# Kernel optimization log

Hardware: AMD Instinct MI355X
Metric: run time of the kernel (lower is better)

## Reference

```python
import jax, jax.numpy as jnp
import numpy as np

N = 50000      # nodes
E = 400000     # edges (before self-loops)
G = 256        # graphs in batch
H = 2          # attention heads
C = 100        # out channels per head
F_IN = 336
SLOPE = 0.2    # PyG GATConv default negative_slope


def setup_inputs() -> dict:
    key = jax.random.key(0)
    ks = jax.random.split(key, 32)
    inp = {}
    inp['x'] = jax.random.normal(ks[0], (N, F_IN), dtype=jnp.float32)
    inp['edge_index'] = jax.random.randint(ks[1], (2, E), 0, N, dtype=jnp.int32)
    inp['batch'] = jnp.sort(jax.random.randint(ks[2], (N,), 0, G, dtype=jnp.int32))
    dims = [F_IN, 200, 200, 200, 200]
    k = 3
    for i in range(5):
        d = dims[i]
        inp[f'W{i+1}'] = jax.random.normal(ks[k], (d, H * C), dtype=jnp.float32) / float(np.sqrt(d)); k += 1
        inp[f'asrc{i+1}'] = jax.random.normal(ks[k], (H, C), dtype=jnp.float32) * 0.1; k += 1
        inp[f'adst{i+1}'] = jax.random.normal(ks[k], (H, C), dtype=jnp.float32) * 0.1; k += 1
        inp[f'bc{i+1}'] = jnp.zeros((H * C,), jnp.float32)
    for i, (a, b) in enumerate([(200, 100), (100, 100), (100, 29)]):
        inp[f'lw{i+1}'] = jax.random.normal(ks[k], (a, b), dtype=jnp.float32) / float(np.sqrt(a)); k += 1
        inp[f'lb{i+1}'] = jnp.zeros((b,), jnp.float32)
    return inp


def _gat(x, src, dst, W, a_s, a_d, b):
    # PyG GATConv (concat=True): per-head linear, additive attention,
    # softmax over incoming edges per destination node, weighted sum.
    h = (x @ W).reshape(-1, H, C)                      # [N,H,C]
    es = jnp.einsum('nhc,hc->nh', h, a_s)              # [N,H] src scores
    ed = jnp.einsum('nhc,hc->nh', h, a_d)              # [N,H] dst scores
    e = jax.nn.leaky_relu(es[src] + ed[dst], SLOPE)    # [E+N,H]
    m = jax.ops.segment_max(e, dst, num_segments=N)    # per-dest max (stable softmax)
    p = jnp.exp(e - m[dst])
    s = jax.ops.segment_sum(p, dst, num_segments=N)
    alpha = p / (s[dst] + 1e-16)                       # [E+N,H]
    msg = alpha[:, :, None] * h[src]                   # [E+N,H,C]
    out = jax.ops.segment_sum(msg, dst, num_segments=N)
    return out.reshape(-1, H * C) + b


def reference(x, edge_index, batch,
              W1, asrc1, adst1, bc1, W2, asrc2, adst2, bc2,
              W3, asrc3, adst3, bc3, W4, asrc4, adst4, bc4,
              W5, asrc5, adst5, bc5,
              lw1, lb1, lw2, lb2, lw3, lb3):
    loop = jnp.arange(N, dtype=edge_index.dtype)       # self-loops (PyG default)
    src = jnp.concatenate([edge_index[0], loop])
    dst = jnp.concatenate([edge_index[1], loop])
    for W, a_s, a_d, b in [(W1, asrc1, adst1, bc1), (W2, asrc2, adst2, bc2),
                           (W3, asrc3, adst3, bc3), (W4, asrc4, adst4, bc4),
                           (W5, asrc5, adst5, bc5)]:
        x = jax.nn.relu(_gat(x, src, dst, W, a_s, a_d, b))
    # global mean pool over nodes of each graph
    sums = jax.ops.segment_sum(x, batch, num_segments=G)
    cnt = jax.ops.segment_sum(jnp.ones((N, 1), x.dtype), batch, num_segments=G)
    x = sums / jnp.maximum(cnt, 1.0)
    x = jax.nn.relu(x @ lw1 + lb1)
    x = jax.nn.relu(x @ lw2 + lb2)
    return x @ lw3 + lb3
```

## Files before the change

### kernel.cpp

```cpp
#include <hip/hip_runtime.h>
#include <hip/hip_bf16.h>
#include <math.h>

#define F_IN   336
#define HC     200
#define Cch    100
#define SLOPE  0.2f
#define SCAN_BS 256

#define NPAD   224
#define KP0    352
#define KP1    224

using short8   = __attribute__((ext_vector_type(8))) short;
using float4v  = __attribute__((ext_vector_type(4))) float;
using ushort4v = __attribute__((ext_vector_type(4))) unsigned short;
using float2v  = __attribute__((ext_vector_type(2))) float;

typedef __attribute__((address_space(1))) const void GASV;
typedef __attribute__((address_space(3))) void LASV;

__device__ inline unsigned short rne_bf16(float v) {
    unsigned int u = __float_as_uint(v);
    return (unsigned short)((u + 0x7fffu + ((u >> 16) & 1u)) >> 16);
}
__device__ inline void split_bf(float v, unsigned short& hi, unsigned short& lo) {
    hi = rne_bf16(v);
    float hv = __uint_as_float(((unsigned int)hi) << 16);
    lo = rne_bf16(v - hv);
}

__device__ inline unsigned int enc_f32(float f) {
    unsigned int u = __float_as_uint(f);
    return (u & 0x80000000u) ? ~u : (u | 0x80000000u);
}
__device__ inline float dec_f32(unsigned int e) {
    return __uint_as_float((e & 0x80000000u) ? (e ^ 0x80000000u) : ~e);
}

__global__ void init_deg(int* deg, unsigned int* gmax, int n) {
    int i = blockIdx.x * 256 + threadIdx.x;
    if (i < n) deg[i] = 1;
    if (i < 10) gmax[i] = 0x007FFFFFu;
}

__global__ void count_deg(const int* __restrict__ dst, int* deg, int e) {
    int i = blockIdx.x * 256 + threadIdx.x;
    if (i < e) atomicAdd(&deg[dst[i]], 1);
}

__global__ void scan_block(const int* __restrict__ deg, int* incl, int* bsums, int n) {
    __shared__ int sm[SCAN_BS];
    int i = blockIdx.x * SCAN_BS + threadIdx.x;
    int v = (i < n) ? deg[i] : 0;
    sm[threadIdx.x] = v;
    __syncthreads();
    for (int off = 1; off < SCAN_BS; off <<= 1) {
        int t = (threadIdx.x >= off) ? sm[threadIdx.x - off] : 0;
        __syncthreads();
        sm[threadIdx.x] += t;
        __syncthreads();
    }
    if (i < n) incl[i] = sm[threadIdx.x];
    if (threadIdx.x == SCAN_BS - 1) bsums[blockIdx.x] = sm[threadIdx.x];
}

__global__ void scan_sums(int* bsums, int nb) {
    __shared__ int sm[SCAN_BS];
    int v = (threadIdx.x < nb) ? bsums[threadIdx.x] : 0;
    sm[threadIdx.x] = v;
    __syncthreads();
    for (int off = 1; off < SCAN_BS; off <<= 1) {
        int t = (threadIdx.x >= off) ? sm[threadIdx.x - off] : 0;
        __syncthreads();
        sm[threadIdx.x] += t;
        __syncthreads();
    }
    if (threadIdx.x < nb) bsums[threadIdx.x] = sm[threadIdx.x] - v;
}

__global__ void scan_final(const int* __restrict__ incl, const int* __restrict__ deg,
                           const int* __restrict__ bsums, int* row_ptr, int* cursor, int n) {
    int i = blockIdx.x * SCAN_BS + threadIdx.x;
    if (i < n) {
        int inc = incl[i] + bsums[i / SCAN_BS];
        int ex  = inc - deg[i];
        row_ptr[i] = ex;
        cursor[i]  = ex;
        if (i == n - 1) row_ptr[n] = inc;
    }
}

__global__ void fill_csr(const int* __restrict__ src, const int* __restrict__ dst,
                         int* cursor, int* col_src, int e, int n) {
    int i = blockIdx.x * 256 + threadIdx.x;
    int te = e + n;
    if (i >= te) return;
    int s, d;
    if (i < e) { s = src[i]; d = dst[i]; }
    else       { s = i - e;  d = i - e; }
    int pos = atomicAdd(&cursor[d], 1);
    col_src[pos] = s;
}

__global__ void conv_x(const float* __restrict__ x, unsigned short* __restrict__ Ah,
                       unsigned short* __restrict__ Al, int n_nodes) {
    const int GPR = KP0 / 4;
    int i = blockIdx.x * 256 + threadIdx.x;
    int tot = n_nodes * GPR;
    if (i >= tot) return;
    int row = i / GPR, g4 = i - row * GPR;
    int col = g4 * 4;
    float4v v = {0.f, 0.f, 0.f, 0.f};
    if (col < F_IN) v = *(const float4v*)(x + (size_t)row * F_IN + col);
    ushort4v hv, lv;
    split_bf(v.x, ((unsigned short*)&hv)[0], ((unsigned short*)&lv)[0]);
    split_bf(v.y, ((unsigned short*)&hv)[1], ((unsigned short*)&lv)[1]);
    split_bf(v.z, ((unsigned short*)&hv)[2], ((unsigned short*)&lv)[2]);
    split_bf(v.w, ((unsigned short*)&hv)[3], ((unsigned short*)&lv)[3]);
    size_t b = (size_t)row * KP0 + col;
    *(ushort4v*)(Ah + b) = hv;
    *(ushort4v*)(Al + b) = lv;
}

__global__ void conv_w_all(const float* __restrict__ W0, const float* __restrict__ W1,
                           const float* __restrict__ W2, const float* __restrict__ W3,
                           const float* __restrict__ W4,
                           unsigned short* __restrict__ Bh, unsigned short* __restrict__ Bl) {
    const int SZ0 = NPAD * KP0, SZ = NPAD * KP1;
    const int TOT = SZ0 + 4 * SZ;
    int i = blockIdx.x * 256 + threadIdx.x;
    if (i >= TOT) return;
    const float* W; int Kp, K, idx;
    if (i < SZ0) { W = W0; Kp = KP0; K = F_IN; idx = i; }
    else {
        int j = i - SZ0; int l = j / SZ; idx = j - l * SZ;
        W = (l == 0) ? W1 : (l == 1) ? W2 : (l == 2) ? W3 : W4;
        Kp = KP1; K = HC;
    }
    int n = idx / Kp, k = idx - n * Kp;
    float v = (n < HC && k < K) ? W[(size_t)k * HC + n] : 0.f;
    unsigned short hi, lo;
    split_bf(v, hi, lo);
    Bh[i] = hi; Bl[i] = lo;
}

#define LBUF 18432
__global__ __launch_bounds__(256, 2) void gemm_split(
    const unsigned short* __restrict__ Ah, const unsigned short* __restrict__ Al,
    const unsigned short* __restrict__ Bh, const unsigned short* __restrict__ Bl,
    const float* __restrict__ asrc, const float* __restrict__ adst,
    float* __restrict__ h, float* __restrict__ es, float* __restrict__ ed,
    unsigned int* __restrict__ gmax,
    int M, int Kp)
{
    __shared__ unsigned short Ls[2][LBUF];
    __shared__ float sc[64][4];
    int tid  = threadIdx.x;
    int wave = tid >> 6, lane = tid & 63;
    int quad = lane >> 4, l16 = lane & 15;
    int wm = (wave >> 1) * 32;
    int wn = (wave & 1) * 112;
    int r0 = blockIdx.x * 64;

    ((float*)sc)[tid] = 0.f;

    const unsigned short* gp[9];
    unsigned lof[9];
    {
        int r16 = lane >> 2;
        int cl  = (lane & 3) ^ ((lane >> 3) & 3);
#pragma unroll
        for (int j = 0; j < 9; j++) {
            int c = wave * 9 + j;
            if (c < 8) {
                int s = c >> 2, rb = (c & 3) * 16;
                int gr = r0 + rb + r16; if (gr >= M) gr = M - 1;
                gp[j]  = (s ? Al : Ah) + (size_t)gr * Kp + cl * 8;
                lof[j] = s * 2048 + rb * 32;
            } else {
                int cb = c - 8;
                int s = (cb >= 14) ? 1 : 0, rb = (cb - s * 14) * 16;
                gp[j]  = (s ? Bl : Bh) + (size_t)(rb + r16) * Kp + cl * 8;
                lof[j] = 4096 + s * 7168 + rb * 32;
            }
        }
    }

    float4v acc[2][7];
#pragma unroll
    for (int mt = 0; mt < 2; mt++)
#pragma unroll
        for (int nt = 0; nt < 7; nt++)
            acc[mt][nt] = (float4v){0.f, 0.f, 0.f, 0.f};

#pragma unroll
    for (int j = 0; j < 9; j++)
        __builtin_amdgcn_global_load_lds((GASV*)(gp[j]), (LASV*)(&Ls[0][0] + lof[j]), 16, 0, 0);
    __syncthreads();

    for (int k0 = 0; k0 < Kp; k0 += 32) {
        int cur = (k0 >> 5) & 1;
        int kn  = k0 + 32;
        if (kn < Kp) {
            unsigned short* lb = &Ls[cur ^ 1][0];
#pragma unroll
            for (int j = 0; j < 9; j++)
                __builtin_amdgcn_global_load_lds((GASV*)(gp[j] + kn), (LASV*)(lb + lof[j]), 16, 0, 0);
        }

        const unsigned short* Lc = &Ls[cur][0];
        short8 a_h[2], a_l[2];
#pragma unroll
        for (int mt = 0; mt < 2; mt++) {
            int row = wm + mt * 16 + l16;
            int cph = (quad ^ ((row >> 1) & 3)) * 8;
            a_h[mt] = *(const short8*)(Lc + row * 32 + cph);
            a_l[mt] = *(const short8*)(Lc + 2048 + row * 32 + cph);
        }
#pragma unroll
        for (int nt = 0; nt < 7; nt++) {
            int row = wn + nt * 16 + l16;
            int cph = (quad ^ ((row >> 1) & 3)) * 8;
            short8 b_h = *(const short8*)(Lc + 4096 + row * 32 + cph);
            short8 b_l = *(const short8*)(Lc + 11264 + row * 32 + cph);
#pragma unroll
            for (int mt = 0; mt < 2; mt++) {
                acc[mt][nt] = __builtin_amdgcn_mfma_f32_16x16x32_bf16(a_h[mt], b_h, acc[mt][nt], 0, 0, 0);
                acc[mt][nt] = __builtin_amdgcn_mfma_f32_16x16x32_bf16(a_h[mt], b_l, acc[mt][nt], 0, 0, 0);
                acc[mt][nt] = __builtin_amdgcn_mfma_f32_16x16x32_bf16(a_l[mt], b_h, acc[mt][nt], 0, 0, 0);
            }
        }
        __syncthreads();
    }

    float asc[7], adc[7];
    bool  vld[7];
    bool  hd1[7];
#pragma unroll
    for (int nt = 0; nt < 7; nt++) {
        int col = wn + nt * 16 + l16;
        vld[nt] = col < HC;
        hd1[nt] = col >= Cch;
        asc[nt] = vld[nt] ? asrc[col] : 0.f;
        adc[nt] = vld[nt] ? adst[col] : 0.f;
    }

#pragma unroll
    for (int mt = 0; mt < 2; mt++) {
        float p[4][4];
#pragma unroll
        for (int r = 0; r < 4; r++)
#pragma unroll
            for (int t = 0; t < 4; t++) p[r][t] = 0.f;
#pragma unroll
        for (int nt = 0; nt < 7; nt++) {
            int col = wn + nt * 16 + l16;
#pragma unroll
            for (int r = 0; r < 4; r++) {
                float v = acc[mt][nt][r];
                int grow = r0 + wm + mt * 16 + quad * 4 + r;
                if (vld[nt] && grow < M) h[(size_t)grow * HC + col] = v;
                float va = v * asc[nt], vd = v * adc[nt];
                p[r][0] += hd1[nt] ? 0.f : va;
                p[r][1] += hd1[nt] ? va  : 0.f;
                p[r][2] += hd1[nt] ? 0.f : vd;
                p[r][3] += hd1[nt] ? vd  : 0.f;
            }
        }
#pragma unroll
        for (int off = 1; off < 16; off <<= 1)
#pragma unroll
            for (int r = 0; r < 4; r++)
#pragma unroll
                for (int t = 0; t < 4; t++)
                    p[r][t] += __shfl_xor(p[r][t], off);
        if (l16 == 0) {
            int lrow = wm + mt * 16 + quad * 4;
#pragma unroll
            for (int r = 0; r < 4; r++)
#pragma unroll
                for (int t = 0; t < 4; t++)
                    atomicAdd(&sc[lrow + r][t], p[r][t]);
        }
    }
    __syncthreads();
    if (tid < 64) {
        int grow = r0 + tid;
        bool v = grow < M;
        float e0v = v ? sc[tid][0] : -INFINITY;
        float e1v = v ? sc[tid][1] : -INFINITY;
        if (v) {
            es[grow * 2 + 0] = e0v;
            es[grow * 2 + 1] = e1v;
            ed[grow * 2 + 0] = sc[tid][2];
            ed[grow * 2 + 1] = sc[tid][3];
        }
#pragma unroll
        for (int off = 1; off < 64; off <<= 1) {
            e0v = fmaxf(e0v, __shfl_xor(e0v, off));
            e1v = fmaxf(e1v, __shfl_xor(e1v, off));
        }
        if (tid == 0) {
            atomicMax(&gmax[0], enc_f32(e0v));
            atomicMax(&gmax[1], enc_f32(e1v));
        }
    }
}

template<bool WF, bool WB>
__global__ __launch_bounds__(256) void gat_gather(
    const float* __restrict__ h, const float* __restrict__ es, const float* __restrict__ ed,
    const unsigned int* __restrict__ gmax,
    const int* __restrict__ row_ptr, const int* __restrict__ col_src,
    const float* __restrict__ bias, float* __restrict__ outF,
    unsigned short* __restrict__ oh, unsigned short* __restrict__ ol, int n_nodes)
{
    int wave = threadIdx.x >> 6, lane = threadIdx.x & 63;
    int n = blockIdx.x * 4 + wave;
    if (n >= n_nodes) return;
    int e0 = row_ptr[n], e1 = row_ptr[n + 1];
    bool act  = lane < 50;
    int  hsel = (lane >= 25) ? 1 : 0;
    float ed0 = ed[n * 2], ed1 = ed[n * 2 + 1];
    float gm0 = dec_f32(gmax[0]), gm1 = dec_f32(gmax[1]);
    float t0 = gm0 + ed0, t1 = gm1 + ed1;
    float mb0 = t0 > 0.f ? t0 : SLOPE * t0;
    float mb1 = t1 > 0.f ? t1 : SLOPE * t1;

    float l0 = 0.f, l1 = 0.f;
    float4v a0 = {0.f, 0.f, 0.f, 0.f}, a1 = {0.f, 0.f, 0.f, 0.f};
    float4v a2 = {0.f, 0.f, 0.f, 0.f}, a3 = {0.f, 0.f, 0.f, 0.f};

    for (int cbase = e0; cbase < e1; cbase += 64) {
        int cnt = e1 - cbase; if (cnt > 64) cnt = 64;
        int   sidx = 0;
        float px = 0.f, py = 0.f;
        if (lane < cnt) {
            sidx = col_src[cbase + lane];
            float2v q = *(const float2v*)&es[sidx * 2];
            float s0 = q.x + ed0, s1 = q.y + ed1;
            s0 = s0 > 0.f ? s0 : SLOPE * s0;
            s1 = s1 > 0.f ? s1 : SLOPE * s1;
            px = __expf(s0 - mb0);
            py = __expf(s1 - mb1);
            l0 += px; l1 += py;
        }
        int j = 0;
        for (; j + 4 <= cnt; j += 4) {
            int s0 = __shfl(sidx, j + 0), s1 = __shfl(sidx, j + 1);
            int s2 = __shfl(sidx, j + 2), s3 = __shfl(sidx, j + 3);
            float x0 = __shfl(px, j + 0), y0 = __shfl(py, j + 0);
            float x1 = __shfl(px, j + 1), y1 = __shfl(py, j + 1);
            float x2 = __shfl(px, j + 2), y2 = __shfl(py, j + 2);
            float x3 = __shfl(px, j + 3), y3 = __shfl(py, j + 3);
            float p0 = hsel ? y0 : x0;
            float p1 = hsel ? y1 : x1;
            float p2 = hsel ? y2 : x2;
            float p3 = hsel ? y3 : x3;
            if (act) {
                float4v v0 = *(const float4v*)(h + (size_t)s0 * HC + lane * 4);
                float4v v1 = *(const float4v*)(h + (size_t)s1 * HC + lane * 4);
                float4v v2 = *(const float4v*)(h + (size_t)s2 * HC + lane * 4);
                float4v v3 = *(const float4v*)(h + (size_t)s3 * HC + lane * 4);
                a0.x += p0 * v0.x; a0.y += p0 * v0.y; a0.z += p0 * v0.z; a0.w += p0 * v0.w;
                a1.x += p1 * v1.x; a1.y += p1 * v1.y; a1.z += p1 * v1.z; a1.w += p1 * v1.w;
                a2.x += p2 * v2.x; a2.y += p2 * v2.y; a2.z += p2 * v2.z; a2.w += p2 * v2.w;
                a3.x += p3 * v3.x; a3.y += p3 * v3.y; a3.z += p3 * v3.z; a3.w += p3 * v3.w;
            }
        }
        for (; j < cnt; j++) {
            int s0 = __shfl(sidx, j);
            float x0 = __shfl(px, j), y0 = __shfl(py, j);
            float p0 = hsel ? y0 : x0;
            if (act) {
                float4v v0 = *(const float4v*)(h + (size_t)s0 * HC + lane * 4);
                a0.x += p0 * v0.x; a0.y += p0 * v0.y; a0.z += p0 * v0.z; a0.w += p0 * v0.w;
            }
        }
    }
#pragma unroll
    for (int off = 1; off < 64; off <<= 1) {
        l0 += __shfl_xor(l0, off);
        l1 += __shfl_xor(l1, off);
    }

    float4v acc;
    acc.x = (a0.x + a1.x) + (a2.x + a3.x);
    acc.y = (a0.y + a1.y) + (a2.y + a3.y);
    acc.z = (a0.z + a1.z) + (a2.z + a3.z);
    acc.w = (a0.w + a1.w) + (a2.w + a3.w);

    float li = 1.f / ((hsel ? l1 : l0) + 1e-33f);
    if (act) {
        float4v bb = *(const float4v*)(bias + lane * 4);
        float4v r;
        r.x = fmaxf(acc.x * li + bb.x, 0.f);
        r.y = fmaxf(acc.y * li + bb.y, 0.f);
        r.z = fmaxf(acc.z * li + bb.z, 0.f);
        r.w = fmaxf(acc.w * li + bb.w, 0.f);
        if (WF) {
            __builtin_nontemporal_store(r, (float4v*)(outF + (size_t)n * HC + lane * 4));
        }
        if (WB) {
            ushort4v hv, lv;
            split_bf(r.x, ((unsigned short*)&hv)[0], ((unsigned short*)&lv)[0]);
            split_bf(r.y, ((unsigned short*)&hv)[1], ((unsigned short*)&lv)[1]);
            split_bf(r.z, ((unsigned short*)&hv)[2], ((unsigned short*)&lv)[2]);
            split_bf(r.w, ((unsigned short*)&hv)[3], ((unsigned short*)&lv)[3]);
            size_t b = (size_t)n * NPAD + lane * 4;
            __builtin_nontemporal_store(hv, (ushort4v*)(oh + b));
            __builtin_nontemporal_store(lv, (ushort4v*)(ol + b));
        }
    } else if (WB && lane < 56) {
        ushort4v z = {0, 0, 0, 0};
        size_t b = (size_t)n * NPAD + lane * 4;
        __builtin_nontemporal_store(z, (ushort4v*)(oh + b));
        __builtin_nontemporal_store(z, (ushort4v*)(ol + b));
    }
}

__global__ void bounds_zero(const int* __restrict__ batch, int* gstart,
                            float* pool, int n, int g) {
    int i = blockIdx.x * 256 + threadIdx.x;
    if (i < g * HC) pool[i] = 0.f;
    if (i >= n) return;
    int b = batch[i];
    int bp = (i == 0) ? -1 : batch[i - 1];
    for (int q = bp + 1; q <= b; q++) gstart[q] = i;
    if (i == n - 1) for (int q = b + 1; q <= g; q++) gstart[q] = n;
}

__global__ __launch_bounds__(256) void pool_part(
    const float* __restrict__ x, const int* __restrict__ batch,
    float* __restrict__ pool, int n_nodes)
{
    int wave = threadIdx.x >> 6, lane = threadIdx.x & 63;
    int base = (blockIdx.x * 4 + wave) * 16;
    if (base >= n_nodes) return;
    bool act = lane < 50;
    int end = base + 16; if (end > n_nodes) end = n_nodes;
    float4v acc = {0.f, 0.f, 0.f, 0.f};
    int curg = batch[base];
    for (int n = base; n < end; n++) {
        int g = batch[n];
        if (g != curg) {
            if (act) {
                float* pp = pool + (size_t)curg * HC + lane * 4;
                atomicAdd(pp + 0, acc.x); atomicAdd(pp + 1, acc.y);
                atomicAdd(pp + 2, acc.z); atomicAdd(pp + 3, acc.w);
            }
            acc = (float4v){0.f, 0.f, 0.f, 0.f};
            curg = g;
        }
        if (act) {
            float4v v = *(const float4v*)(x + (size_t)n * HC + lane * 4);
            acc.x += v.x; acc.y += v.y; acc.z += v.z; acc.w += v.w;
        }
    }
    if (act) {
        float* pp = pool + (size_t)curg * HC + lane * 4;
        atomicAdd(pp + 0, acc.x); atomicAdd(pp + 1, acc.y);
        atomicAdd(pp + 2, acc.z); atomicAdd(pp + 3, acc.w);
    }
}

__global__ __launch_bounds__(128) void mlp_head(
    const float* __restrict__ pool, const int* __restrict__ gstart,
    const float* __restrict__ lw1, const float* __restrict__ lb1,
    const float* __restrict__ lw2, const float* __restrict__ lb2,
    const float* __restrict__ lw3, const float* __restrict__ lb3,
    float* __restrict__ out)
{
    __shared__ float xa[200];
    __shared__ float xb[100];
    __shared__ float xc[100];
    int g = blockIdx.x, t = threadIdx.x;
    float inv = 1.f / fmaxf((float)(gstart[g + 1] - gstart[g]), 1.f);
    for (int k = t; k < 200; k += 128) xa[k] = pool[g * 200 + k] * inv;
    __syncthreads();
    if (t < 100) {
        float s = lb1[t];
        for (int k = 0; k < 200; k++) s = fmaf(xa[k], lw1[k * 100 + t], s);
        xb[t] = fmaxf(s, 0.f);
    }
    __syncthreads();
    if (t < 100) {
        float s = lb2[t];
        for (int k = 0; k < 100; k++) s = fmaf(xb[k], lw2[k * 100 + t], s);
        xc[t] = fmaxf(s, 0.f);
    }
    __syncthreads();
    if (t < 29) {
        float s = lb3[t];
        for (int k = 0; k < 100; k++) s = fmaf(xc[k], lw3[k * 29 + t], s);
        out[g * 29 + t] = s;
    }
}

extern "C" void kernel_launch(void* const* d_in, const int* in_sizes, int n_in,
                              void* d_out, int out_size, void* d_ws, size_t ws_size,
                              hipStream_t stream) {
    const float* x     = (const float*)d_in[0];
    const int*   ei    = (const int*)d_in[1];
    const int*   batch = (const int*)d_in[2];
    const float *W[5], *asrc[5], *adst[5], *bc[5];
    for (int i = 0; i < 5; i++) {
        W[i]    = (const float*)d_in[3 + i * 4];
        asrc[i] = (const float*)d_in[4 + i * 4];
        adst[i] = (const float*)d_in[5 + i * 4];
        bc[i]   = (const float*)d_in[6 + i * 4];
    }
    const float* lw1 = (const float*)d_in[23];
    const float* lb1 = (const float*)d_in[24];
    const float* lw2 = (const float*)d_in[25];
    const float* lb2 = (const float*)d_in[26];
    const float* lw3 = (const float*)d_in[27];
    const float* lb3 = (const float*)d_in[28];
    float* out = (float*)d_out;

    const int N  = in_sizes[0] / F_IN;
    const int E  = in_sizes[1] / 2;
    const int G  = out_size / 29;
    const int TE = E + N;
    const int* esrc = ei;
    const int* edst = ei + E;

    const int WSZ0 = NPAD * KP0;
    const int WSZ  = NPAD * KP1;
    const int WTOT = WSZ0 + 4 * WSZ;

    char* p = (char*)d_ws;
    auto carve = [&](size_t bytes) { void* r = (void*)p; p += ((bytes + 255) / 256) * 256; return r; };
    float*          hbuf = (float*)carve((size_t)N * HC * 4);
    unsigned short* Ah   = (unsigned short*)carve((size_t)N * KP0 * 2);
    unsigned short* Al   = (unsigned short*)carve((size_t)N * KP0 * 2);
    float*          outF = (float*)Ah;
    unsigned short* Wth  = (unsigned short*)carve((size_t)WTOT * 2);
    unsigned short* Wtl  = (unsigned short*)carve((size_t)WTOT * 2);
    float* es_     = (float*)carve((size_t)N * 2 * 4);
    float* ed_     = (float*)carve((size_t)N * 2 * 4);
    unsigned int* gmax5 = (unsigned int*)carve(10 * 4);
    int*   deg     = (int*)carve((size_t)N * 4);
    int*   incl    = (int*)carve((size_t)N * 4);
    int*   bsums   = (int*)carve(SCAN_BS * 4);
    int*   row_ptr = (int*)carve((size_t)(N + 1) * 4);
    int*   cursor  = (int*)carve((size_t)N * 4);
    int*   col_src = (int*)carve((size_t)TE * 4);
    int*   gstart  = (int*)carve((size_t)(G + 1) * 4);
    float* pool    = (float*)carve((size_t)G * HC * 4);

    const int nBlkN   = (N + 255) / 256;
    const int nBlkE   = (E + 255) / 256;
    const int nBlkTE  = (TE + 255) / 256;
    const int nScanB  = (N + SCAN_BS - 1) / SCAN_BS;
    const int nWaveB  = (N + 3) / 4;
    const int nGemmB  = (N + 63) / 64;
    const int nPoolB  = (N + 63) / 64;
    const int nBZ     = (((N > G * HC) ? N : G * HC) + 255) / 256;

    init_deg<<<nBlkN, 256, 0, stream>>>(deg, gmax5, N);
    count_deg<<<nBlkE, 256, 0, stream>>>(edst, deg, E);
    scan_block<<<nScanB, SCAN_BS, 0, stream>>>(deg, incl, bsums, N);
    scan_sums<<<1, SCAN_BS, 0, stream>>>(bsums, nScanB);
    scan_final<<<nScanB, SCAN_BS, 0, stream>>>(incl, deg, bsums, row_ptr, cursor, N);
    fill_csr<<<nBlkTE, 256, 0, stream>>>(esrc, edst, cursor, col_src, E, N);

    conv_x<<<(N * (KP0 / 4) + 255) / 256, 256, 0, stream>>>(x, Ah, Al, N);
    conv_w_all<<<(WTOT + 255) / 256, 256, 0, stream>>>(W[0], W[1], W[2], W[3], W[4], Wth, Wtl);

    for (int L = 0; L < 5; L++) {
        int Kp   = (L == 0) ? KP0 : KP1;
        int woff = (L == 0) ? 0 : WSZ0 + (L - 1) * WSZ;
        gemm_split<<<nGemmB, 256, 0, stream>>>(Ah, Al, Wth + woff, Wtl + woff,
                                               asrc[L], adst[L], hbuf, es_, ed_,
                                               gmax5 + 2 * L, N, Kp);
        if (L < 4)
            gat_gather<false, true><<<nWaveB, 256, 0, stream>>>(hbuf, es_, ed_, gmax5 + 2 * L,
                                                                row_ptr, col_src,
                                                                bc[L], nullptr, Ah, Al, N);
        else
            gat_gather<true, false><<<nWaveB, 256, 0, stream>>>(hbuf, es_, ed_, gmax5 + 2 * L,
                                                                row_ptr, col_src,
                                                                bc[L], outF, nullptr, nullptr, N);
    }

    bounds_zero<<<nBZ, 256, 0, stream>>>(batch, gstart, pool, N, G);
    pool_part<<<nPoolB, 256, 0, stream>>>(outF, batch, pool, N);
    mlp_head<<<G, 128, 0, stream>>>(pool, gstart, lw1, lb1, lw2, lb2, lw3, lb3, out);
}
```

Measured before the change: 835.2 us.

## Enlarge GEMM M-tile to 128 and use triple-buffered LDS prefetch

The split-bf16 GEMM tile grows from 64 to 128 rows per block, so each wave holds 4x7 accumulators and the B tile is reused across twice as many rows. The double-buffered K loop becomes a three-stage LDS ring that prefetches two steps ahead, with explicit vmcnt waits and a single barrier per iteration in place of two __syncthreads. The aim is to hide global-to-LDS latency and cut B reloads, at the cost of higher register and LDS use (launch bounds drop to one block per SM) and fewer blocks in the grid.

```diff
diff --git a/kernel.cpp b/kernel.cpp
--- a/kernel.cpp
+++ b/kernel.cpp
@@ -145,8 +145,13 @@
     Bh[i] = hi; Bl[i] = lo;
 }
 
-#define LBUF 18432
-__global__ __launch_bounds__(256, 2) void gemm_split(
+#define BM   128
+#define AHW  4096
+#define BHW  7168
+#define BBASE 8192
+#define TBUF 22528
+#define CHW  11
+__global__ __launch_bounds__(256, 1) void gemm_split(
     const unsigned short* __restrict__ Ah, const unsigned short* __restrict__ Al,
     const unsigned short* __restrict__ Bh, const unsigned short* __restrict__ Bl,
     const float* __restrict__ asrc, const float* __restrict__ adst,
@@ -154,84 +159,94 @@
     unsigned int* __restrict__ gmax,
     int M, int Kp)
 {
-    __shared__ unsigned short Ls[2][LBUF];
-    __shared__ float sc[64][4];
+    __shared__ unsigned short Ls[3][TBUF];
+    __shared__ float sc[BM][4];
     int tid  = threadIdx.x;
     int wave = tid >> 6, lane = tid & 63;
     int quad = lane >> 4, l16 = lane & 15;
-    int wm = (wave >> 1) * 32;
+    int wm = (wave >> 1) * 64;
     int wn = (wave & 1) * 112;
-    int r0 = blockIdx.x * 64;
+    int r0 = blockIdx.x * BM;
+    int nk = Kp >> 5;
 
     ((float*)sc)[tid] = 0.f;
-
-    const unsigned short* gp[9];
-    unsigned lof[9];
+    ((float*)sc)[tid + 256] = 0.f;
+
+    const unsigned short* gp[CHW];
+    unsigned lof[CHW];
     {
         int r16 = lane >> 2;
         int cl  = (lane & 3) ^ ((lane >> 3) & 3);
 #pragma unroll
-        for (int j = 0; j < 9; j++) {
-            int c = wave * 9 + j;
-            if (c < 8) {
-                int s = c >> 2, rb = (c & 3) * 16;
+        for (int j = 0; j < CHW; j++) {
+            int c = wave * CHW + j;
+            if (c < 16) {
+                int s = c >> 3, rb = (c & 7) * 16;
                 int gr = r0 + rb + r16; if (gr >= M) gr = M - 1;
                 gp[j]  = (s ? Al : Ah) + (size_t)gr * Kp + cl * 8;
-                lof[j] = s * 2048 + rb * 32;
+                lof[j] = s * AHW + rb * 32;
             } else {
-                int cb = c - 8;
+                int cb = c - 16;
                 int s = (cb >= 14) ? 1 : 0, rb = (cb - s * 14) * 16;
                 gp[j]  = (s ? Bl : Bh) + (size_t)(rb + r16) * Kp + cl * 8;
-                lof[j] = 4096 + s * 7168 + rb * 32;
+                lof[j] = BBASE + s * BHW + rb * 32;
             }
         }
     }
 
-    float4v acc[2][7];
-#pragma unroll
-    for (int mt = 0; mt < 2; mt++)
+    float4v acc[4][7];
+#pragma unroll
+    for (int mt = 0; mt < 4; mt++)
 #pragma unroll
         for (int nt = 0; nt < 7; nt++)
             acc[mt][nt] = (float4v){0.f, 0.f, 0.f, 0.f};
 
 #pragma unroll
-    for (int j = 0; j < 9; j++)
+    for (int j = 0; j < CHW; j++)
         __builtin_amdgcn_global_load_lds((GASV*)(gp[j]), (LASV*)(&Ls[0][0] + lof[j]), 16, 0, 0);
-    __syncthreads();
-
-    for (int k0 = 0; k0 < Kp; k0 += 32) {
-        int cur = (k0 >> 5) & 1;
-        int kn  = k0 + 32;
-        if (kn < Kp) {
-            unsigned short* lb = &Ls[cur ^ 1][0];
-#pragma unroll
-            for (int j = 0; j < 9; j++)
-                __builtin_amdgcn_global_load_lds((GASV*)(gp[j] + kn), (LASV*)(lb + lof[j]), 16, 0, 0);
+#pragma unroll
+    for (int j = 0; j < CHW; j++)
+        __builtin_amdgcn_global_load_lds((GASV*)(gp[j] + 32), (LASV*)(&Ls[1][0] + lof[j]), 16, 0, 0);
+
+    int cur = 0;
+    for (int t = 0; t < nk; t++) {
+        if (t + 1 < nk) { asm volatile("s_waitcnt vmcnt(11)" ::: "memory"); }
+        else            { asm volatile("s_waitcnt vmcnt(0)"  ::: "memory"); }
+        __builtin_amdgcn_s_barrier();
+        asm volatile("" ::: "memory");
+
+        if (t + 2 < nk) {
+            int pf = cur + 2; if (pf >= 3) pf -= 3;
+            unsigned short* lb = &Ls[pf][0];
+            int koff = (t + 2) * 32;
+#pragma unroll
+            for (int j = 0; j < CHW; j++)
+                __builtin_amdgcn_global_load_lds((GASV*)(gp[j] + koff), (LASV*)(lb + lof[j]), 16, 0, 0);
         }
 
         const unsigned short* Lc = &Ls[cur][0];
-        short8 a_h[2], a_l[2];
-#pragma unroll
-        for (int mt = 0; mt < 2; mt++) {
+        short8 a_h[4], a_l[4];
+#pragma unroll
+        for (int mt = 0; mt < 4; mt++) {
             int row = wm + mt * 16 + l16;
             int cph = (quad ^ ((row >> 1) & 3)) * 8;
             a_h[mt] = *(const short8*)(Lc + row * 32 + cph);
-            a_l[mt] = *(const short8*)(Lc + 2048 + row * 32 + cph);
+            a_l[mt] = *(const short8*)(Lc + AHW + row * 32 + cph);
         }
 #pragma unroll
         for (int nt = 0; nt < 7; nt++) {
             int row = wn + nt * 16 + l16;
             int cph = (quad ^ ((row >> 1) & 3)) * 8;
-            short8 b_h = *(const short8*)(Lc + 4096 + row * 32 + cph);
-            short8 b_l = *(const short8*)(Lc + 11264 + row * 32 + cph);
-#pragma unroll
-            for (int mt = 0; mt < 2; mt++) {
+            short8 b_h = *(const short8*)(Lc + BBASE + row * 32 + cph);
+            short8 b_l = *(const short8*)(Lc + BBASE + BHW + row * 32 + cph);
+#pragma unroll
+            for (int mt = 0; mt < 4; mt++) {
                 acc[mt][nt] = __builtin_amdgcn_mfma_f32_16x16x32_bf16(a_h[mt], b_h, acc[mt][nt], 0, 0, 0);
                 acc[mt][nt] = __builtin_amdgcn_mfma_f32_16x16x32_bf16(a_h[mt], b_l, acc[mt][nt], 0, 0, 0);
                 acc[mt][nt] = __builtin_amdgcn_mfma_f32_16x16x32_bf16(a_l[mt], b_h, acc[mt][nt], 0, 0, 0);
             }
         }
-        __syncthreads();
+        cur = (cur == 2) ? 0 : cur + 1;
     }
 
     float asc[7], adc[7];
@@ -247,7 +262,7 @@
     }
 
 #pragma unroll
-    for (int mt = 0; mt < 2; mt++) {
+    for (int mt = 0; mt < 4; mt++) {
         float p[4][4];
 #pragma unroll
         for (int r = 0; r < 4; r++)
@@ -285,7 +300,7 @@
         }
     }
     __syncthreads();
-    if (tid < 64) {
+    if (tid < BM) {
         int grow = r0 + tid;
         bool v = grow < M;
         float e0v = v ? sc[tid][0] : -INFINITY;
@@ -301,7 +316,7 @@
             e0v = fmaxf(e0v, __shfl_xor(e0v, off));
             e1v = fmaxf(e1v, __shfl_xor(e1v, off));
         }
-        if (tid == 0) {
+        if (lane == 0) {
             atomicMax(&gmax[0], enc_f32(e0v));
             atomicMax(&gmax[1], enc_f32(e1v));
         }
@@ -555,7 +570,7 @@
     const int nBlkTE  = (TE + 255) / 256;
     const int nScanB  = (N + SCAN_BS - 1) / SCAN_BS;
     const int nWaveB  = (N + 3) / 4;
-    const int nGemmB  = (N + 63) / 64;
+    const int nGemmB  = (N + BM - 1) / BM;
     const int nPoolB  = (N + 63) / 64;
     const int nBZ     = (((N > G * HC) ? N : G * HC) + 255) / 256;
 
```

New measurement: 889.8 us. 1.07x slower.

## Retile split-bf16 GEMM to 128x128 blocks with 4-stage async LDS pipeline

Applied to the files above, without the earlier changes.

Reworks the GEMM into 512-thread blocks that each compute a 128-row by 128-column tile, so each row chunk is split across two column-half blocks. K-tile loading becomes a 4-buffer pipeline with explicit vmcnt waits instead of double buffering with a trailing syncthreads. Because the two heads' score dot products now span two blocks, the src/dst score and global max partials are written to separate A/B buffers and summed in the gather kernel. This adds extra score memory traffic and pads the weight matrices to 256 columns, where the second half-block does wasted work on 56 padding columns.

```diff
diff --git a/kernel.cpp b/kernel.cpp
--- a/kernel.cpp
+++ b/kernel.cpp
@@ -9,6 +9,7 @@
 #define SCAN_BS 256
 
 #define NPAD   224
+#define NROWS  256
 #define KP0    352
 #define KP1    224
 
@@ -41,7 +42,7 @@
 __global__ void init_deg(int* deg, unsigned int* gmax, int n) {
     int i = blockIdx.x * 256 + threadIdx.x;
     if (i < n) deg[i] = 1;
-    if (i < 10) gmax[i] = 0x007FFFFFu;
+    if (i < 20) gmax[i] = 0x007FFFFFu;
 }
 
 __global__ void count_deg(const int* __restrict__ dst, int* deg, int e) {
@@ -127,7 +128,7 @@
                            const float* __restrict__ W2, const float* __restrict__ W3,
                            const float* __restrict__ W4,
                            unsigned short* __restrict__ Bh, unsigned short* __restrict__ Bl) {
-    const int SZ0 = NPAD * KP0, SZ = NPAD * KP1;
+    const int SZ0 = NROWS * KP0, SZ = NROWS * KP1;
     const int TOT = SZ0 + 4 * SZ;
     int i = blockIdx.x * 256 + threadIdx.x;
     if (i >= TOT) return;
@@ -145,85 +146,106 @@
     Bh[i] = hi; Bl[i] = lo;
 }
 
-#define LBUF 18432
-__global__ __launch_bounds__(256, 2) void gemm_split(
+#define BMR   128
+#define BNC   128
+#define AHW2  4096
+#define BB2   8192
+#define STG   16384
+__global__ __launch_bounds__(512, 1) void gemm_split(
     const unsigned short* __restrict__ Ah, const unsigned short* __restrict__ Al,
     const unsigned short* __restrict__ Bh, const unsigned short* __restrict__ Bl,
     const float* __restrict__ asrc, const float* __restrict__ adst,
-    float* __restrict__ h, float* __restrict__ es, float* __restrict__ ed,
+    float* __restrict__ h,
+    float* __restrict__ esA, float* __restrict__ esB,
+    float* __restrict__ edA, float* __restrict__ edB,
     unsigned int* __restrict__ gmax,
     int M, int Kp)
 {
-    __shared__ unsigned short Ls[2][LBUF];
-    __shared__ float sc[64][4];
+    __shared__ unsigned short Ls[4][STG];
+    __shared__ float sc[BMR][4];
     int tid  = threadIdx.x;
     int wave = tid >> 6, lane = tid & 63;
     int quad = lane >> 4, l16 = lane & 15;
     int wm = (wave >> 1) * 32;
-    int wn = (wave & 1) * 112;
-    int r0 = blockIdx.x * 64;
+    int wn = (wave & 1) * 64;
+    int bx = blockIdx.x;
+    int half  = bx & 1;
+    int chunk = bx >> 1;
+    int r0 = chunk * BMR;
+    int c0 = half * BNC;
+    int nk = Kp >> 5;
+
+    float* esP = half ? esB : esA;
+    float* edP = half ? edB : edA;
 
     ((float*)sc)[tid] = 0.f;
 
-    const unsigned short* gp[9];
-    unsigned lof[9];
+    const unsigned short* gp[4];
+    unsigned lof[4];
     {
         int r16 = lane >> 2;
         int cl  = (lane & 3) ^ ((lane >> 3) & 3);
 #pragma unroll
-        for (int j = 0; j < 9; j++) {
-            int c = wave * 9 + j;
-            if (c < 8) {
-                int s = c >> 2, rb = (c & 3) * 16;
+        for (int j = 0; j < 4; j++) {
+            int c = wave * 4 + j;
+            if (c < 16) {
+                int s = c >> 3, rb = (c & 7) * 16;
                 int gr = r0 + rb + r16; if (gr >= M) gr = M - 1;
                 gp[j]  = (s ? Al : Ah) + (size_t)gr * Kp + cl * 8;
-                lof[j] = s * 2048 + rb * 32;
+                lof[j] = s * AHW2 + rb * 32;
             } else {
-                int cb = c - 8;
-                int s = (cb >= 14) ? 1 : 0, rb = (cb - s * 14) * 16;
-                gp[j]  = (s ? Bl : Bh) + (size_t)(rb + r16) * Kp + cl * 8;
-                lof[j] = 4096 + s * 7168 + rb * 32;
+                int cb = c - 16;
+                int s = cb >> 3, rb = (cb & 7) * 16;
+                gp[j]  = (s ? Bl : Bh) + (size_t)(c0 + rb + r16) * Kp + cl * 8;
+                lof[j] = BB2 + s * AHW2 + rb * 32;
             }
         }
     }
 
-    float4v acc[2][7];
+    float4v acc[2][4];
 #pragma unroll
     for (int mt = 0; mt < 2; mt++)
 #pragma unroll
-        for (int nt = 0; nt < 7; nt++)
+        for (int nt = 0; nt < 4; nt++)
             acc[mt][nt] = (float4v){0.f, 0.f, 0.f, 0.f};
 
 #pragma unroll
-    for (int j = 0; j < 9; j++)
-        __builtin_amdgcn_global_load_lds((GASV*)(gp[j]), (LASV*)(&Ls[0][0] + lof[j]), 16, 0, 0);
-    __syncthreads();
-
-    for (int k0 = 0; k0 < Kp; k0 += 32) {
-        int cur = (k0 >> 5) & 1;
-        int kn  = k0 + 32;
-        if (kn < Kp) {
-            unsigned short* lb = &Ls[cur ^ 1][0];
-#pragma unroll
-            for (int j = 0; j < 9; j++)
-                __builtin_amdgcn_global_load_lds((GASV*)(gp[j] + kn), (LASV*)(lb + lof[j]), 16, 0, 0);
-        }
-
-        const unsigned short* Lc = &Ls[cur][0];
+    for (int tt = 0; tt < 3; tt++)
+#pragma unroll
+        for (int j = 0; j < 4; j++)
+            __builtin_amdgcn_global_load_lds((GASV*)(gp[j] + tt * 32),
+                                             (LASV*)(&Ls[tt][0] + lof[j]), 16, 0, 0);
+
+    for (int t = 0; t < nk; t++) {
+        int rem = nk - 1 - t;
+        if (rem >= 2)      { asm volatile("s_waitcnt vmcnt(8)" ::: "memory"); }
+        else if (rem == 1) { asm volatile("s_waitcnt vmcnt(4)" ::: "memory"); }
+        else               { asm volatile("s_waitcnt vmcnt(0)" ::: "memory"); }
+        __builtin_amdgcn_s_barrier();
+
+        if (t + 3 < nk) {
+            unsigned short* lb = &Ls[(t + 3) & 3][0];
+            int koff = (t + 3) * 32;
+#pragma unroll
+            for (int j = 0; j < 4; j++)
+                __builtin_amdgcn_global_load_lds((GASV*)(gp[j] + koff),
+                                                 (LASV*)(lb + lof[j]), 16, 0, 0);
+        }
+
+        const unsigned short* Lc = &Ls[t & 3][0];
+        int cph = (quad ^ ((l16 >> 1) & 3)) * 8;
         short8 a_h[2], a_l[2];
 #pragma unroll
         for (int mt = 0; mt < 2; mt++) {
             int row = wm + mt * 16 + l16;
-            int cph = (quad ^ ((row >> 1) & 3)) * 8;
             a_h[mt] = *(const short8*)(Lc + row * 32 + cph);
-            a_l[mt] = *(const short8*)(Lc + 2048 + row * 32 + cph);
-        }
-#pragma unroll
-        for (int nt = 0; nt < 7; nt++) {
+            a_l[mt] = *(const short8*)(Lc + AHW2 + row * 32 + cph);
+        }
+#pragma unroll
+        for (int nt = 0; nt < 4; nt++) {
             int row = wn + nt * 16 + l16;
-            int cph = (quad ^ ((row >> 1) & 3)) * 8;
-            short8 b_h = *(const short8*)(Lc + 4096 + row * 32 + cph);
-            short8 b_l = *(const short8*)(Lc + 11264 + row * 32 + cph);
+            short8 b_h = *(const short8*)(Lc + BB2 + row * 32 + cph);
+            short8 b_l = *(const short8*)(Lc + BB2 + AHW2 + row * 32 + cph);
 #pragma unroll
             for (int mt = 0; mt < 2; mt++) {
                 acc[mt][nt] = __builtin_amdgcn_mfma_f32_16x16x32_bf16(a_h[mt], b_h, acc[mt][nt], 0, 0, 0);
@@ -231,19 +253,18 @@
                 acc[mt][nt] = __builtin_amdgcn_mfma_f32_16x16x32_bf16(a_l[mt], b_h, acc[mt][nt], 0, 0, 0);
             }
         }
-        __syncthreads();
-    }
-
-    float asc[7], adc[7];
-    bool  vld[7];
-    bool  hd1[7];
-#pragma unroll
-    for (int nt = 0; nt < 7; nt++) {
-        int col = wn + nt * 16 + l16;
+    }
+
+    float asc4[4], adc4[4];
+    bool  vld[4];
+    bool  hd1[4];
+#pragma unroll
+    for (int nt = 0; nt < 4; nt++) {
+        int col = c0 + wn + nt * 16 + l16;
         vld[nt] = col < HC;
         hd1[nt] = col >= Cch;
-        asc[nt] = vld[nt] ? asrc[col] : 0.f;
-        adc[nt] = vld[nt] ? adst[col] : 0.f;
+        asc4[nt] = vld[nt] ? asrc[col] : 0.f;
+        adc4[nt] = vld[nt] ? adst[col] : 0.f;
     }
 
 #pragma unroll
@@ -254,14 +275,14 @@
 #pragma unroll
             for (int t = 0; t < 4; t++) p[r][t] = 0.f;
 #pragma unroll
-        for (int nt = 0; nt < 7; nt++) {
-            int col = wn + nt * 16 + l16;
+        for (int nt = 0; nt < 4; nt++) {
+            int col = c0 + wn + nt * 16 + l16;
 #pragma unroll
             for (int r = 0; r < 4; r++) {
                 float v = acc[mt][nt][r];
                 int grow = r0 + wm + mt * 16 + quad * 4 + r;
                 if (vld[nt] && grow < M) h[(size_t)grow * HC + col] = v;
-                float va = v * asc[nt], vd = v * adc[nt];
+                float va = v * asc4[nt], vd = v * adc4[nt];
                 p[r][0] += hd1[nt] ? 0.f : va;
                 p[r][1] += hd1[nt] ? va  : 0.f;
                 p[r][2] += hd1[nt] ? 0.f : vd;
@@ -285,32 +306,34 @@
         }
     }
     __syncthreads();
-    if (tid < 64) {
+    if (tid < BMR) {
         int grow = r0 + tid;
         bool v = grow < M;
         float e0v = v ? sc[tid][0] : -INFINITY;
         float e1v = v ? sc[tid][1] : -INFINITY;
         if (v) {
-            es[grow * 2 + 0] = e0v;
-            es[grow * 2 + 1] = e1v;
-            ed[grow * 2 + 0] = sc[tid][2];
-            ed[grow * 2 + 1] = sc[tid][3];
+            esP[grow * 2 + 0] = e0v;
+            esP[grow * 2 + 1] = e1v;
+            edP[grow * 2 + 0] = sc[tid][2];
+            edP[grow * 2 + 1] = sc[tid][3];
         }
 #pragma unroll
         for (int off = 1; off < 64; off <<= 1) {
             e0v = fmaxf(e0v, __shfl_xor(e0v, off));
             e1v = fmaxf(e1v, __shfl_xor(e1v, off));
         }
-        if (tid == 0) {
-            atomicMax(&gmax[0], enc_f32(e0v));
-            atomicMax(&gmax[1], enc_f32(e1v));
+        if (lane == 0) {
+            atomicMax(&gmax[half * 2 + 0], enc_f32(e0v));
+            atomicMax(&gmax[half * 2 + 1], enc_f32(e1v));
         }
     }
 }
 
 template<bool WF, bool WB>
 __global__ __launch_bounds__(256) void gat_gather(
-    const float* __restrict__ h, const float* __restrict__ es, const float* __restrict__ ed,
+    const float* __restrict__ h,
+    const float* __restrict__ esA, const float* __restrict__ esB,
+    const float* __restrict__ edA, const float* __restrict__ edB,
     const unsigned int* __restrict__ gmax,
     const int* __restrict__ row_ptr, const int* __restrict__ col_src,
     const float* __restrict__ bias, float* __restrict__ outF,
@@ -322,8 +345,10 @@
     int e0 = row_ptr[n], e1 = row_ptr[n + 1];
     bool act  = lane < 50;
     int  hsel = (lane >= 25) ? 1 : 0;
-    float ed0 = ed[n * 2], ed1 = ed[n * 2 + 1];
-    float gm0 = dec_f32(gmax[0]), gm1 = dec_f32(gmax[1]);
+    float ed0 = edA[n * 2]     + edB[n * 2];
+    float ed1 = edA[n * 2 + 1] + edB[n * 2 + 1];
+    float gm0 = dec_f32(gmax[0]) + dec_f32(gmax[2]);
+    float gm1 = dec_f32(gmax[1]) + dec_f32(gmax[3]);
     float t0 = gm0 + ed0, t1 = gm1 + ed1;
     float mb0 = t0 > 0.f ? t0 : SLOPE * t0;
     float mb1 = t1 > 0.f ? t1 : SLOPE * t1;
@@ -338,8 +363,9 @@
         float px = 0.f, py = 0.f;
         if (lane < cnt) {
             sidx = col_src[cbase + lane];
-            float2v q = *(const float2v*)&es[sidx * 2];
-            float s0 = q.x + ed0, s1 = q.y + ed1;
+            float2v qa = *(const float2v*)&esA[sidx * 2];
+            float2v qb = *(const float2v*)&esB[sidx * 2];
+            float s0 = qa.x + qb.x + ed0, s1 = qa.y + qb.y + ed1;
             s0 = s0 > 0.f ? s0 : SLOPE * s0;
             s1 = s1 > 0.f ? s1 : SLOPE * s1;
             px = __expf(s0 - mb0);
@@ -526,8 +552,8 @@
     const int* esrc = ei;
     const int* edst = ei + E;
 
-    const int WSZ0 = NPAD * KP0;
-    const int WSZ  = NPAD * KP1;
+    const int WSZ0 = NROWS * KP0;
+    const int WSZ  = NROWS * KP1;
     const int WTOT = WSZ0 + 4 * WSZ;
 
     char* p = (char*)d_ws;
@@ -538,9 +564,11 @@
     float*          outF = (float*)Ah;
     unsigned short* Wth  = (unsigned short*)carve((size_t)WTOT * 2);
     unsigned short* Wtl  = (unsigned short*)carve((size_t)WTOT * 2);
-    float* es_     = (float*)carve((size_t)N * 2 * 4);
-    float* ed_     = (float*)carve((size_t)N * 2 * 4);
-    unsigned int* gmax5 = (unsigned int*)carve(10 * 4);
+    float* esA_    = (float*)carve((size_t)N * 2 * 4);
+    float* esB_    = (float*)carve((size_t)N * 2 * 4);
+    float* edA_    = (float*)carve((size_t)N * 2 * 4);
+    float* edB_    = (float*)carve((size_t)N * 2 * 4);
+    unsigned int* gmax5 = (unsigned int*)carve(20 * 4);
     int*   deg     = (int*)carve((size_t)N * 4);
     int*   incl    = (int*)carve((size_t)N * 4);
     int*   bsums   = (int*)carve(SCAN_BS * 4);
@@ -555,7 +583,7 @@
     const int nBlkTE  = (TE + 255) / 256;
     const int nScanB  = (N + SCAN_BS - 1) / SCAN_BS;
     const int nWaveB  = (N + 3) / 4;
-    const int nGemmB  = (N + 63) / 64;
+    const int nGemmB  = ((N + BMR - 1) / BMR) * 2;
     const int nPoolB  = (N + 63) / 64;
     const int nBZ     = (((N > G * HC) ? N : G * HC) + 255) / 256;
 
@@ -572,15 +600,18 @@
     for (int L = 0; L < 5; L++) {
         int Kp   = (L == 0) ? KP0 : KP1;
         int woff = (L == 0) ? 0 : WSZ0 + (L - 1) * WSZ;
-        gemm_split<<<nGemmB, 256, 0, stream>>>(Ah, Al, Wth + woff, Wtl + woff,
-                                               asrc[L], adst[L], hbuf, es_, ed_,
-                                               gmax5 + 2 * L, N, Kp);
+        gemm_split<<<nGemmB, 512, 0, stream>>>(Ah, Al, Wth + woff, Wtl + woff,
+                                               asrc[L], adst[L], hbuf,
+                                               esA_, esB_, edA_, edB_,
+                                               gmax5 + 4 * L, N, Kp);
         if (L < 4)
-            gat_gather<false, true><<<nWaveB, 256, 0, stream>>>(hbuf, es_, ed_, gmax5 + 2 * L,
+            gat_gather<false, true><<<nWaveB, 256, 0, stream>>>(hbuf, esA_, esB_, edA_, edB_,
+                                                                gmax5 + 4 * L,
                                                                 row_ptr, col_src,
                                                                 bc[L], nullptr, Ah, Al, N);
         else
-            gat_gather<true, false><<<nWaveB, 256, 0, stream>>>(hbuf, es_, ed_, gmax5 + 2 * L,
+            gat_gather<true, false><<<nWaveB, 256, 0, stream>>>(hbuf, esA_, esB_, edA_, edB_,
+                                                                gmax5 + 4 * L,
                                                                 row_ptr, col_src,
                                                                 bc[L], outF, nullptr, nullptr, N);
     }
```

Measured after the change: 1.031 ms. +23.5%, slower.
